# Kernel tuning notes

Measured on AMD Instinct MI355X. Metric: run time of the kernel, lower is better.

Reference implementation:

```python
import jax, jax.numpy as jnp
import numpy as np

N_NODES = 100000
N_EDGES = 3200000
IN_CH, HID, OUT_CH = 602, 16, 41


def setup_inputs() -> dict:
    key = jax.random.key(0)
    ks = jax.random.split(key, 5)
    x = jax.random.normal(ks[0], (N_NODES, IN_CH), dtype=jnp.float32)
    edge_index = jax.random.randint(ks[1], (2, N_EDGES), 0, N_NODES, dtype=jnp.int32)
    # glorot init for weights, zeros for biases (matches reset_parameters)
    W1 = jax.random.normal(ks[2], (IN_CH, HID), dtype=jnp.float32) * np.sqrt(2.0 / (IN_CH + HID))
    b1 = jnp.zeros((HID,), dtype=jnp.float32)
    W2 = jax.random.normal(ks[3], (HID, OUT_CH), dtype=jnp.float32) * np.sqrt(2.0 / (HID + OUT_CH))
    b2 = jnp.zeros((OUT_CH,), dtype=jnp.float32)
    return {"x": x, "edge_index": edge_index, "W1": W1, "b1": b1, "W2": W2, "b2": b2}


def _sage_conv(x, src, dst, W, b, n_nodes):
    # linear transform first (16-wide), then gather-scatter-mean over edges
    h = x @ W                                   # [N, out]
    msg = h[src]                                # [E, out] gather of source nodes
    agg = jax.ops.segment_sum(msg, dst, num_segments=n_nodes)          # [N, out]
    cnt = jax.ops.segment_sum(jnp.ones((src.shape[0], 1), h.dtype), dst,
                              num_segments=n_nodes)                     # [N, 1]
    mean = agg / jnp.maximum(cnt, 1.0)          # scatter-mean (0 for isolated nodes)
    return mean + b


def reference(x, edge_index, W1, b1, W2, b2):
    src, dst = edge_index[0], edge_index[1]     # source_to_target flow
    n = x.shape[0]
    h = jax.nn.relu(_sage_conv(x, src, dst, W1, b1, n))
    # F.dropout(training=False) -> identity (inference mode)
    out = _sage_conv(h, src, dst, W2, b2, n)
    return jax.nn.log_softmax(out, axis=1)
```

## Files before the change

kernel.cpp:

```cpp
#include <hip/hip_runtime.h>
#include <cmath>

#define NN 100000
#define NE 3200000
#define CIN 602
#define CH 16
#define COUT 41
#define TB 128
#define KTL 32

#define NPB 128
#define NB  ((NN + NPB - 1) / NPB)
#define EPC 32
#define ECHUNK (256 * EPC)
#define EB  ((NE + ECHUNK - 1) / ECHUNK)

__device__ float g_h1[NN * CH];
__device__ float g_h1b[NN * CH];
__device__ float g_agg2[NN * CH];
__device__ int   g_deg[NN];
__device__ int   g_rs[NN + 1];
__device__ int   g_csr[NE];
__device__ int2  g_pair[NE];
__device__ int   g_cnt[NB * EB];
__device__ int   g_colsum[NB];
__device__ int   g_bbase[NB + 1];

__device__ __forceinline__ int clamp_node(int v) {
    return v < 0 ? 0 : (v >= NN ? NN - 1 : v);
}

__global__ __launch_bounds__(256) void fallback_zero_out_k(float* __restrict__ out, int n) {
    int i = blockIdx.x * blockDim.x + threadIdx.x;
    if (i < n) out[i] = 0.0f;
}

__global__ __launch_bounds__(256) void count_k(const int* __restrict__ ei) {
    __shared__ int h[NB];
    const int t = threadIdx.x;
    for (int i = t; i < NB; i += 256) h[i] = 0;
    __syncthreads();
    const int base = blockIdx.x * ECHUNK;
#pragma unroll
    for (int j = 0; j < EPC; ++j) {
        int e = base + j * 256 + t;
        if (e < NE) {
            int d = clamp_node(ei[NE + e]);
            atomicAdd(&h[d >> 7], 1);
        }
    }
    __syncthreads();
    for (int i = t; i < NB; i += 256) g_cnt[i * EB + blockIdx.x] = h[i];
}

__global__ __launch_bounds__(256) void scanA_k() {
    const int b = blockIdx.x;
    const int t = threadIdx.x;
    __shared__ int a[512];
    __shared__ int sh[256];
    a[t]       = (t < EB)       ? g_cnt[b * EB + t]       : 0;
    a[t + 256] = (t + 256 < EB) ? g_cnt[b * EB + t + 256] : 0;
    __syncthreads();
    int e0 = a[2 * t], e1 = a[2 * t + 1];
    int sum = e0 + e1;
    sh[t] = sum;
    __syncthreads();
    for (int off = 1; off < 256; off <<= 1) {
        int v = (t >= off) ? sh[t - off] : 0;
        __syncthreads();
        sh[t] += v;
        __syncthreads();
    }
    int run = sh[t] - sum;
    if (2 * t < EB)     g_cnt[b * EB + 2 * t]     = run;
    if (2 * t + 1 < EB) g_cnt[b * EB + 2 * t + 1] = run + e0;
    if (t == 255) g_colsum[b] = sh[255];
}

__global__ __launch_bounds__(1024) void scanB_k() {
    const int t = threadIdx.x;
    __shared__ int sh[1024];
    int v = (t < NB) ? g_colsum[t] : 0;
    sh[t] = v;
    __syncthreads();
    for (int off = 1; off < 1024; off <<= 1) {
        int u = (t >= off) ? sh[t - off] : 0;
        __syncthreads();
        sh[t] += u;
        __syncthreads();
    }
    if (t < NB) g_bbase[t] = sh[t] - v;
    if (t == 1023) {
        g_bbase[NB] = sh[1023];
        g_rs[NN]    = sh[1023];
    }
}

__global__ __launch_bounds__(256) void scatter_k(const int* __restrict__ ei) {
    __shared__ int lb[NB];
    const int t = threadIdx.x;
    for (int i = t; i < NB; i += 256)
        lb[i] = g_bbase[i] + g_cnt[i * EB + blockIdx.x];
    __syncthreads();
    const int base = blockIdx.x * ECHUNK;
#pragma unroll
    for (int j = 0; j < EPC; ++j) {
        int e = base + j * 256 + t;
        if (e < NE) {
            int s = clamp_node(ei[e]);
            int d = clamp_node(ei[NE + e]);
            int p = atomicAdd(&lb[d >> 7], 1);
            g_pair[p] = make_int2(s, d);
        }
    }
}

__global__ __launch_bounds__(256) void build_k() {
    const int b = blockIdx.x;
    const int t = threadIdx.x;
    const int n0 = b * NPB;
    const int e0 = g_bbase[b], e1 = g_bbase[b + 1];
    __shared__ int ldeg[NPB];
    __shared__ int lrs[NPB + 1];
    __shared__ int lcur[NPB];
    if (t < NPB) ldeg[t] = 0;
    __syncthreads();
    for (int e = e0 + t; e < e1; e += 256) {
        int2 p = g_pair[e];
        atomicAdd(&ldeg[p.y - n0], 1);
    }
    __syncthreads();
    if (t == 0) {
        int run = 0;
        for (int i = 0; i < NPB; ++i) { lrs[i] = run; run += ldeg[i]; }
        lrs[NPB] = run;
    }
    __syncthreads();
    if (t < NPB) {
        int node = n0 + t;
        if (node < NN) {
            g_rs[node]  = e0 + lrs[t];
            g_deg[node] = ldeg[t];
        }
        lcur[t] = lrs[t];
    }
    __syncthreads();
    for (int e = e0 + t; e < e1; e += 256) {
        int2 p = g_pair[e];
        int r = atomicAdd(&lcur[p.y - n0], 1);
        g_csr[e0 + r] = p.x;
    }
}

__global__ __launch_bounds__(TB) void gemm1_k(const float* __restrict__ x,
                                              const float* __restrict__ W1) {
    __shared__ float xs[KTL][TB + 1];
    const int t = threadIdx.x;
    const int l  = t & 15;
    const int rg = t >> 4;
    const int row0 = blockIdx.x * TB;
    const int row  = row0 + t;

    float acc[CH];
#pragma unroll
    for (int c = 0; c < CH; ++c) acc[c] = 0.f;

    float2 ld[16];

    auto stage_load = [&](int kb) {
#pragma unroll
        for (int p = 0; p < 16; ++p) {
            int rgl = row0 + rg + 8 * p;
            ld[p] = (rgl < NN)
                ? *reinterpret_cast<const float2*>(x + (size_t)rgl * CIN + kb + 2 * l)
                : make_float2(0.f, 0.f);
        }
    };
    auto stage_load_ep = [&]() {
#pragma unroll
        for (int p = 0; p < 16; ++p) {
            int rgl = row0 + rg + 8 * p;
            ld[p] = (rgl < NN && l <= 12)
                ? *reinterpret_cast<const float2*>(x + (size_t)rgl * CIN + 576 + 2 * l)
                : make_float2(0.f, 0.f);
        }
    };
    auto stage_store = [&]() {
#pragma unroll
        for (int p = 0; p < 16; ++p) {
            int rl = rg + 8 * p;
            xs[2 * l][rl]     = ld[p].x;
            xs[2 * l + 1][rl] = ld[p].y;
        }
    };

    stage_load(0);
    for (int ti = 0; ti < 18; ++ti) {
        stage_store();
        __syncthreads();
        if (ti < 17) stage_load(KTL * (ti + 1)); else stage_load_ep();
        const int kb = KTL * ti;
#pragma unroll 8
        for (int kk = 0; kk < KTL; ++kk) {
            float xv = xs[kk][t];
            const float4* w4 = reinterpret_cast<const float4*>(W1 + (size_t)(kb + kk) * CH);
            float4 w0 = w4[0], w1 = w4[1], w2 = w4[2], w3 = w4[3];
            acc[0]  += xv * w0.x; acc[1]  += xv * w0.y; acc[2]  += xv * w0.z; acc[3]  += xv * w0.w;
            acc[4]  += xv * w1.x; acc[5]  += xv * w1.y; acc[6]  += xv * w1.z; acc[7]  += xv * w1.w;
            acc[8]  += xv * w2.x; acc[9]  += xv * w2.y; acc[10] += xv * w2.z; acc[11] += xv * w2.w;
            acc[12] += xv * w3.x; acc[13] += xv * w3.y; acc[14] += xv * w3.z; acc[15] += xv * w3.w;
        }
        __syncthreads();
    }
    stage_store();
    __syncthreads();
#pragma unroll 13
    for (int kk = 0; kk < 26; ++kk) {
        float xv = xs[kk][t];
        const float4* w4 = reinterpret_cast<const float4*>(W1 + (size_t)(576 + kk) * CH);
        float4 w0 = w4[0], w1 = w4[1], w2 = w4[2], w3 = w4[3];
        acc[0]  += xv * w0.x; acc[1]  += xv * w0.y; acc[2]  += xv * w0.z; acc[3]  += xv * w0.w;
        acc[4]  += xv * w1.x; acc[5]  += xv * w1.y; acc[6]  += xv * w1.z; acc[7]  += xv * w1.w;
        acc[8]  += xv * w2.x; acc[9]  += xv * w2.y; acc[10] += xv * w2.z; acc[11] += xv * w2.w;
        acc[12] += xv * w3.x; acc[13] += xv * w3.y; acc[14] += xv * w3.z; acc[15] += xv * w3.w;
    }

    if (row < NN) {
        float4* hp = reinterpret_cast<float4*>(g_h1 + (size_t)row * CH);
        hp[0] = make_float4(acc[0],  acc[1],  acc[2],  acc[3]);
        hp[1] = make_float4(acc[4],  acc[5],  acc[6],  acc[7]);
        hp[2] = make_float4(acc[8],  acc[9],  acc[10], acc[11]);
        hp[3] = make_float4(acc[12], acc[13], acc[14], acc[15]);
    }
}

__global__ __launch_bounds__(256) void gather1_k(const float* __restrict__ b1) {
    int tid = blockIdx.x * blockDim.x + threadIdx.x;
    if (tid >= NN * 4) return;
    int node = tid >> 2, q = tid & 3;
    int start = g_rs[node], end = g_rs[node + 1];
    float4 acc = make_float4(0.f, 0.f, 0.f, 0.f);
    int e = start;
    for (; e + 1 < end; e += 2) {
        int s0 = g_csr[e], s1 = g_csr[e + 1];
        float4 a = *reinterpret_cast<const float4*>(&g_h1[(size_t)s0 * CH + (q << 2)]);
        float4 b = *reinterpret_cast<const float4*>(&g_h1[(size_t)s1 * CH + (q << 2)]);
        acc.x += a.x + b.x; acc.y += a.y + b.y;
        acc.z += a.z + b.z; acc.w += a.w + b.w;
    }
    if (e < end) {
        int s0 = g_csr[e];
        float4 a = *reinterpret_cast<const float4*>(&g_h1[(size_t)s0 * CH + (q << 2)]);
        acc.x += a.x; acc.y += a.y; acc.z += a.z; acc.w += a.w;
    }
    float inv = 1.0f / fmaxf((float)(end - start), 1.0f);
    float4 bv = reinterpret_cast<const float4*>(b1)[q];
    float4 r;
    r.x = fmaxf(acc.x * inv + bv.x, 0.f);
    r.y = fmaxf(acc.y * inv + bv.y, 0.f);
    r.z = fmaxf(acc.z * inv + bv.z, 0.f);
    r.w = fmaxf(acc.w * inv + bv.w, 0.f);
    reinterpret_cast<float4*>(g_h1b)[(size_t)node * 4 + q] = r;
}

__global__ __launch_bounds__(256) void gather2_k() {
    int tid = blockIdx.x * blockDim.x + threadIdx.x;
    if (tid >= NN * 4) return;
    int node = tid >> 2, q = tid & 3;
    int start = g_rs[node], end = g_rs[node + 1];
    float4 acc = make_float4(0.f, 0.f, 0.f, 0.f);
    int e = start;
    for (; e + 1 < end; e += 2) {
        int s0 = g_csr[e], s1 = g_csr[e + 1];
        float4 a = *reinterpret_cast<const float4*>(&g_h1b[(size_t)s0 * CH + (q << 2)]);
        float4 b = *reinterpret_cast<const float4*>(&g_h1b[(size_t)s1 * CH + (q << 2)]);
        acc.x += a.x + b.x; acc.y += a.y + b.y;
        acc.z += a.z + b.z; acc.w += a.w + b.w;
    }
    if (e < end) {
        int s0 = g_csr[e];
        float4 a = *reinterpret_cast<const float4*>(&g_h1b[(size_t)s0 * CH + (q << 2)]);
        acc.x += a.x; acc.y += a.y; acc.z += a.z; acc.w += a.w;
    }
    reinterpret_cast<float4*>(g_agg2)[(size_t)node * 4 + q] = acc;
}

__global__ __launch_bounds__(256) void final_k(const float* __restrict__ W2,
                                               const float* __restrict__ b2,
                                               float* __restrict__ out) {
    int gtid = blockIdx.x * blockDim.x + threadIdx.x;
    int node = gtid >> 6;
    int lane = gtid & 63;
    if (node >= NN) return;
    float inv = 1.0f / fmaxf((float)g_deg[node], 1.0f);
    float o = -INFINITY;
    if (lane < COUT) {
        float s = 0.f;
#pragma unroll
        for (int k = 0; k < CH; ++k)
            s += g_agg2[(size_t)node * CH + k] * W2[k * COUT + lane];
        o = s * inv + b2[lane];
    }
    float m = o;
#pragma unroll
    for (int off = 32; off > 0; off >>= 1) m = fmaxf(m, __shfl_xor(m, off, 64));
    float ex = (lane < COUT) ? expf(o - m) : 0.0f;
    float ssum = ex;
#pragma unroll
    for (int off = 32; off > 0; off >>= 1) ssum += __shfl_xor(ssum, off, 64);
    if (lane < COUT) out[(size_t)node * COUT + lane] = o - m - logf(ssum);
}

extern "C" void kernel_launch(void* const* d_in, const int* in_sizes, int n_in,
                              void* d_out, int out_size, void* d_ws, size_t ws_size,
                              hipStream_t stream) {
    (void)d_ws; (void)ws_size;
    float* out = (float*)d_out;

    const int expect[6] = {NN * CIN, 2 * NE, CIN * CH, CH, CH * COUT, COUT};
    bool ok = (n_in >= 6) && (out_size == NN * COUT);
    if (ok) {
        for (int i = 0; i < 6; ++i)
            if (in_sizes[i] != expect[i]) { ok = false; break; }
    }
    if (!ok) {
        int n = out_size > 0 ? out_size : 1;
        fallback_zero_out_k<<<(n + 255) / 256, 256, 0, stream>>>(out, n);
        return;
    }

    const float* x  = (const float*)d_in[0];
    const int*   ei = (const int*)d_in[1];
    const float* W1 = (const float*)d_in[2];
    const float* b1 = (const float*)d_in[3];
    const float* W2 = (const float*)d_in[4];
    const float* b2 = (const float*)d_in[5];

    count_k  <<<EB, 256, 0, stream>>>(ei);
    scanA_k  <<<NB, 256, 0, stream>>>();
    scanB_k  <<<1, 1024, 0, stream>>>();
    scatter_k<<<EB, 256, 0, stream>>>(ei);
    build_k  <<<NB, 256, 0, stream>>>();
    gemm1_k  <<<(NN + TB - 1) / TB, TB, 0, stream>>>(x, W1);
    gather1_k<<<(NN * 4 + 255) / 256, 256, 0, stream>>>(b1);
    gather2_k<<<(NN * 4 + 255) / 256, 256, 0, stream>>>();
    final_k  <<<(NN * 64 + 255) / 256, 256, 0, stream>>>(W2, b2, out);
}
```

Before: 666.1 us.

## Use one wavefront per node for gathers and fuse layer-2 gather with final

```diff
diff --git a/kernel.cpp b/kernel.cpp
--- a/kernel.cpp
+++ b/kernel.cpp
@@ -17,8 +17,6 @@
 
 __device__ float g_h1[NN * CH];
 __device__ float g_h1b[NN * CH];
-__device__ float g_agg2[NN * CH];
-__device__ int   g_deg[NN];
 __device__ int   g_rs[NN + 1];
 __device__ int   g_csr[NE];
 __device__ int2  g_pair[NE];
@@ -138,10 +136,7 @@
     __syncthreads();
     if (t < NPB) {
         int node = n0 + t;
-        if (node < NN) {
-            g_rs[node]  = e0 + lrs[t];
-            g_deg[node] = ldeg[t];
-        }
+        if (node < NN) g_rs[node] = e0 + lrs[t];
         lcur[t] = lrs[t];
     }
     __syncthreads();
@@ -235,14 +230,16 @@
 }
 
 __global__ __launch_bounds__(256) void gather1_k(const float* __restrict__ b1) {
-    int tid = blockIdx.x * blockDim.x + threadIdx.x;
-    if (tid >= NN * 4) return;
-    int node = tid >> 2, q = tid & 3;
+    int gtid = blockIdx.x * blockDim.x + threadIdx.x;
+    int node = gtid >> 6;
+    int l    = gtid & 63;
+    int q    = l & 3;
+    int es   = l >> 2;
     int start = g_rs[node], end = g_rs[node + 1];
     float4 acc = make_float4(0.f, 0.f, 0.f, 0.f);
-    int e = start;
-    for (; e + 1 < end; e += 2) {
-        int s0 = g_csr[e], s1 = g_csr[e + 1];
+    int e = start + es;
+    for (; e + 16 < end; e += 32) {
+        int s0 = g_csr[e], s1 = g_csr[e + 16];
         float4 a = *reinterpret_cast<const float4*>(&g_h1[(size_t)s0 * CH + (q << 2)]);
         float4 b = *reinterpret_cast<const float4*>(&g_h1[(size_t)s1 * CH + (q << 2)]);
         acc.x += a.x + b.x; acc.y += a.y + b.y;
@@ -253,25 +250,43 @@
         float4 a = *reinterpret_cast<const float4*>(&g_h1[(size_t)s0 * CH + (q << 2)]);
         acc.x += a.x; acc.y += a.y; acc.z += a.z; acc.w += a.w;
     }
-    float inv = 1.0f / fmaxf((float)(end - start), 1.0f);
-    float4 bv = reinterpret_cast<const float4*>(b1)[q];
-    float4 r;
-    r.x = fmaxf(acc.x * inv + bv.x, 0.f);
-    r.y = fmaxf(acc.y * inv + bv.y, 0.f);
-    r.z = fmaxf(acc.z * inv + bv.z, 0.f);
-    r.w = fmaxf(acc.w * inv + bv.w, 0.f);
-    reinterpret_cast<float4*>(g_h1b)[(size_t)node * 4 + q] = r;
-}
-
-__global__ __launch_bounds__(256) void gather2_k() {
-    int tid = blockIdx.x * blockDim.x + threadIdx.x;
-    if (tid >= NN * 4) return;
-    int node = tid >> 2, q = tid & 3;
+#pragma unroll
+    for (int off = 4; off < 64; off <<= 1) {
+        acc.x += __shfl_xor(acc.x, off, 64);
+        acc.y += __shfl_xor(acc.y, off, 64);
+        acc.z += __shfl_xor(acc.z, off, 64);
+        acc.w += __shfl_xor(acc.w, off, 64);
+    }
+    if (l < 4) {
+        float inv = 1.0f / fmaxf((float)(end - start), 1.0f);
+        float4 bv = reinterpret_cast<const float4*>(b1)[l];
+        float4 r;
+        r.x = fmaxf(acc.x * inv + bv.x, 0.f);
+        r.y = fmaxf(acc.y * inv + bv.y, 0.f);
+        r.z = fmaxf(acc.z * inv + bv.z, 0.f);
+        r.w = fmaxf(acc.w * inv + bv.w, 0.f);
+        reinterpret_cast<float4*>(g_h1b)[(size_t)node * 4 + l] = r;
+    }
+}
+
+__global__ __launch_bounds__(256) void g2final_k(const float* __restrict__ W2,
+                                                 const float* __restrict__ b2,
+                                                 float* __restrict__ out) {
+    __shared__ float w2s[CH * COUT];
+    const int t = threadIdx.x;
+    for (int i = t; i < CH * COUT; i += 256) w2s[i] = W2[i];
+    __syncthreads();
+
+    int gtid = blockIdx.x * blockDim.x + t;
+    int node = gtid >> 6;
+    int l    = gtid & 63;
+    int q    = l & 3;
+    int es   = l >> 2;
     int start = g_rs[node], end = g_rs[node + 1];
     float4 acc = make_float4(0.f, 0.f, 0.f, 0.f);
-    int e = start;
-    for (; e + 1 < end; e += 2) {
-        int s0 = g_csr[e], s1 = g_csr[e + 1];
+    int e = start + es;
+    for (; e + 16 < end; e += 32) {
+        int s0 = g_csr[e], s1 = g_csr[e + 16];
         float4 a = *reinterpret_cast<const float4*>(&g_h1b[(size_t)s0 * CH + (q << 2)]);
         float4 b = *reinterpret_cast<const float4*>(&g_h1b[(size_t)s1 * CH + (q << 2)]);
         acc.x += a.x + b.x; acc.y += a.y + b.y;
@@ -282,33 +297,36 @@
         float4 a = *reinterpret_cast<const float4*>(&g_h1b[(size_t)s0 * CH + (q << 2)]);
         acc.x += a.x; acc.y += a.y; acc.z += a.z; acc.w += a.w;
     }
-    reinterpret_cast<float4*>(g_agg2)[(size_t)node * 4 + q] = acc;
-}
-
-__global__ __launch_bounds__(256) void final_k(const float* __restrict__ W2,
-                                               const float* __restrict__ b2,
-                                               float* __restrict__ out) {
-    int gtid = blockIdx.x * blockDim.x + threadIdx.x;
-    int node = gtid >> 6;
-    int lane = gtid & 63;
-    if (node >= NN) return;
-    float inv = 1.0f / fmaxf((float)g_deg[node], 1.0f);
+#pragma unroll
+    for (int off = 4; off < 64; off <<= 1) {
+        acc.x += __shfl_xor(acc.x, off, 64);
+        acc.y += __shfl_xor(acc.y, off, 64);
+        acc.z += __shfl_xor(acc.z, off, 64);
+        acc.w += __shfl_xor(acc.w, off, 64);
+    }
+    float a16[CH];
+#pragma unroll
+    for (int k = 0; k < CH; ++k) {
+        float comp = ((k & 3) == 0) ? acc.x : ((k & 3) == 1) ? acc.y
+                   : ((k & 3) == 2) ? acc.z : acc.w;
+        a16[k] = __shfl(comp, k >> 2, 64);
+    }
+    float inv = 1.0f / fmaxf((float)(end - start), 1.0f);
     float o = -INFINITY;
-    if (lane < COUT) {
+    if (l < COUT) {
         float s = 0.f;
 #pragma unroll
-        for (int k = 0; k < CH; ++k)
-            s += g_agg2[(size_t)node * CH + k] * W2[k * COUT + lane];
-        o = s * inv + b2[lane];
+        for (int k = 0; k < CH; ++k) s += a16[k] * w2s[k * COUT + l];
+        o = s * inv + b2[l];
     }
     float m = o;
 #pragma unroll
     for (int off = 32; off > 0; off >>= 1) m = fmaxf(m, __shfl_xor(m, off, 64));
-    float ex = (lane < COUT) ? expf(o - m) : 0.0f;
+    float ex = (l < COUT) ? expf(o - m) : 0.0f;
     float ssum = ex;
 #pragma unroll
     for (int off = 32; off > 0; off >>= 1) ssum += __shfl_xor(ssum, off, 64);
-    if (lane < COUT) out[(size_t)node * COUT + lane] = o - m - logf(ssum);
+    if (l < COUT) out[(size_t)node * COUT + l] = o - m - logf(ssum);
 }
 
 extern "C" void kernel_launch(void* const* d_in, const int* in_sizes, int n_in,
@@ -336,13 +354,14 @@
     const float* W2 = (const float*)d_in[4];
     const float* b2 = (const float*)d_in[5];
 
+    const int WAVE_BLKS = (NN * 64 + 255) / 256;
+
     count_k  <<<EB, 256, 0, stream>>>(ei);
     scanA_k  <<<NB, 256, 0, stream>>>();
     scanB_k  <<<1, 1024, 0, stream>>>();
     scatter_k<<<EB, 256, 0, stream>>>(ei);
     build_k  <<<NB, 256, 0, stream>>>();
     gemm1_k  <<<(NN + TB - 1) / TB, TB, 0, stream>>>(x, W1);
-    gather1_k<<<(NN * 4 + 255) / 256, 256, 0, stream>>>(b1);
-    gather2_k<<<(NN * 4 + 255) / 256, 256, 0, stream>>>();
-    final_k  <<<(NN * 64 + 255) / 256, 256, 0, stream>>>(W2, b2, out);
-}
+    gather1_k<<<WAVE_BLKS, 256, 0, stream>>>(b1);
+    g2final_k<<<WAVE_BLKS, 256, 0, stream>>>(W2, b2, out);
+}
```

Result: faster. 616.3 us (-7.5%).
